# Kernel tuning notes

Measured on AMD Instinct MI355X. Metric: run time of the kernel, lower is better.

The kernel has to match this reference:

```python
import jax, jax.numpy as jnp
import numpy as np
from jax import lax

B, H, W, C = 64, 224, 224, 3
FLAT = 27040  # 52*52*10 after localization convs/pools


def conv_relu(x, w, b):
    y = lax.conv_general_dilated(x, w, (1, 1), 'VALID',
                                 dimension_numbers=('NHWC', 'HWIO', 'NHWC'))
    return jax.nn.relu(y + b)


def maxpool2(x):
    return lax.reduce_window(x, -jnp.inf, lax.max, (1, 2, 2, 1), (1, 2, 2, 1), 'VALID')


def affine_grid(h, w, theta):
    # normalized coords in [-1, 1]
    xt, yt = jnp.meshgrid(jnp.linspace(-1.0, 1.0, w), jnp.linspace(-1.0, 1.0, h))
    grid = jnp.stack([xt.ravel(), yt.ravel(), jnp.ones(h * w, theta.dtype)], 0)  # (3, h*w)
    g = jnp.einsum('bij,jp->bip', theta, grid)  # (B, 2, h*w)
    return g.reshape(-1, 2, h, w)


def bilinear_sampler(img, xs, ys):
    # xs, ys: (B, h, w) in [-1, 1]; img: (B, H, W, C)
    max_y, max_x = img.shape[1] - 1, img.shape[2] - 1
    x = 0.5 * (xs + 1.0) * max_x
    y = 0.5 * (ys + 1.0) * max_y
    x0 = jnp.clip(jnp.floor(x).astype(jnp.int32), 0, max_x)
    x1 = jnp.clip(x0 + 1, 0, max_x)
    y0 = jnp.clip(jnp.floor(y).astype(jnp.int32), 0, max_y)
    y1 = jnp.clip(y0 + 1, 0, max_y)
    b = jnp.arange(img.shape[0])[:, None, None]
    Ia = img[b, y0, x0]  # (B,h,w,C)
    Ib = img[b, y1, x0]
    Ic = img[b, y0, x1]
    Id = img[b, y1, x1]
    x0f, x1f = x0.astype(x.dtype), x1.astype(x.dtype)
    y0f, y1f = y0.astype(y.dtype), y1.astype(y.dtype)
    wa = ((x1f - x) * (y1f - y))[..., None]
    wb = ((x1f - x) * (y - y0f))[..., None]
    wc = ((x - x0f) * (y1f - y))[..., None]
    wd = ((x - x0f) * (y - y0f))[..., None]
    return wa * Ia + wb * Ib + wc * Ic + wd * Id


def setup_inputs() -> dict:
    key = jax.random.key(0)
    ks = jax.random.split(key, 6)
    inputs = jax.random.normal(ks[0], (B, H, W, C), jnp.float32)
    conv1_w = jax.random.normal(ks[1], (7, 7, 3, 8), jnp.float32) * (2.0 / (7 * 7 * 3)) ** 0.5
    conv1_b = jnp.zeros((8,), jnp.float32)
    conv2_w = jax.random.normal(ks[2], (5, 5, 8, 10), jnp.float32) * (2.0 / (5 * 5 * 8)) ** 0.5
    conv2_b = jnp.zeros((10,), jnp.float32)
    fc1_w = jax.random.normal(ks[3], (FLAT, 32), jnp.float32) * (2.0 / FLAT) ** 0.5
    fc1_b = jnp.zeros((32,), jnp.float32)
    fc2_w = jax.random.normal(ks[4], (32, 6), jnp.float32) * 0.01
    fc2_b = jnp.array([1, 0, 0, 0, 1, 0], jnp.float32)  # identity affine init
    return dict(inputs=inputs, conv1_w=conv1_w, conv1_b=conv1_b,
                conv2_w=conv2_w, conv2_b=conv2_b, fc1_w=fc1_w, fc1_b=fc1_b,
                fc2_w=fc2_w, fc2_b=fc2_b)


def reference(inputs, conv1_w, conv1_b, conv2_w, conv2_b, fc1_w, fc1_b, fc2_w, fc2_b):
    xs = maxpool2(conv_relu(inputs, conv1_w, conv1_b))
    xs = maxpool2(conv_relu(xs, conv2_w, conv2_b))
    xs = xs.reshape(xs.shape[0], -1)  # (B, 27040)
    h1 = jax.nn.relu(xs @ fc1_w + fc1_b)
    theta = (h1 @ fc2_w + fc2_b).reshape(-1, 2, 3)
    grid = affine_grid(H, W, theta)  # (B, 2, H, W)
    return bilinear_sampler(inputs, grid[:, 0], grid[:, 1])
```

## Files before the change

kernel.cpp:

```cpp
#include <hip/hip_runtime.h>


__global__ __launch_bounds__(256) void k_wcvt(
    const float* __restrict__ w1, const float* __restrict__ b1,
    const float* __restrict__ w2, const float* __restrict__ b2,
    double* __restrict__ wd) {
  int t = blockIdx.x * 256 + threadIdx.x;
  if (t < 1176) wd[t] = (double)w1[t];
  else if (t < 1184) wd[t] = (double)b1[t - 1176];
  else if (t < 3184) wd[t] = (double)w2[t - 1184];
  else if (t < 3194) wd[t] = (double)b2[t - 3184];
}

__global__ __launch_bounds__(448) void k_conv1(
    const float* __restrict__ in, const double* __restrict__ wd,
    double* __restrict__ out) {
  __shared__ float win[14 * 672];

  int g = blockIdx.x & 7;
  int i = blockIdx.x >> 3;
  int b = g * 8 + i / 28;
  int tile = i % 28;
  int py0 = 4 * tile;
  int r0 = 8 * tile;

  {
    const float* ibb = in + (size_t)b * 150528;
    for (int idx = threadIdx.x; idx < 14 * 168; idx += 448) {
      int rr = idx / 168, c4 = idx % 168;
      int row = min(r0 + rr, 223);
      float4 v = reinterpret_cast<const float4*>(ibb + (size_t)row * 672)[c4];
      reinterpret_cast<float4*>(&win[rr * 672])[c4] = v;
    }
  }
  __syncthreads();

  int t = threadIdx.x;
  int py = py0 + t / 109;
  if (t < 436 && py < 109) {
    int px = t % 109;
    int lrb = 2 * (t / 109);

    double acc[2][2][8];
#pragma unroll
    for (int ii = 0; ii < 2; ++ii)
#pragma unroll
      for (int j = 0; j < 2; ++j)
#pragma unroll
        for (int k = 0; k < 8; ++k) acc[ii][j][k] = 0.0;

    for (int ky = 0; ky < 7; ++ky) {
      const float* r0p = &win[(lrb + ky) * 672 + 6 * px];
      const float* r1p = r0p + 672;
      float a0[24], a1[24];
#pragma unroll
      for (int j = 0; j < 12; ++j) {
        float2 u = reinterpret_cast<const float2*>(r0p)[j];
        a0[2 * j] = u.x; a0[2 * j + 1] = u.y;
        float2 v = reinterpret_cast<const float2*>(r1p)[j];
        a1[2 * j] = v.x; a1[2 * j + 1] = v.y;
      }
      const double* wk = wd + ky * 168;
#pragma unroll
      for (int kx = 0; kx < 7; ++kx) {
#pragma unroll
        for (int c = 0; c < 3; ++c) {
          double v00 = (double)a0[kx * 3 + c];
          double v01 = (double)a0[kx * 3 + 3 + c];
          double v10 = (double)a1[kx * 3 + c];
          double v11 = (double)a1[kx * 3 + 3 + c];
          const double* wp = wk + (kx * 3 + c) * 8;
#pragma unroll
          for (int oc = 0; oc < 8; ++oc) {
            double wv = wp[oc];
            acc[0][0][oc] = fma(v00, wv, acc[0][0][oc]);
            acc[0][1][oc] = fma(v01, wv, acc[0][1][oc]);
            acc[1][0][oc] = fma(v10, wv, acc[1][0][oc]);
            acc[1][1][oc] = fma(v11, wv, acc[1][1][oc]);
          }
        }
      }
    }

    double* op = out + ((size_t)b * 11881 + (size_t)py * 109 + px) * 8;
#pragma unroll
    for (int oc = 0; oc < 8; ++oc) {
      double m = fmax(fmax(acc[0][0][oc], acc[0][1][oc]),
                      fmax(acc[1][0][oc], acc[1][1][oc]));
      op[oc] = fmax(m + wd[1176 + oc], 0.0);
    }
  }
}

__global__ __launch_bounds__(512) void k_conv2(
    const double* __restrict__ in, const double* __restrict__ wd2,
    double* __restrict__ out) {
  __shared__ double win2[4 * 12 * 2 * 56];

  int g = blockIdx.x & 7;
  int i = blockIdx.x >> 3;
  int b = g * 8 + i / 13;
  int tile = i % 13;
  int py0 = 4 * tile;
  int r0 = 8 * tile;

  int t = threadIdx.x;
  int oh = __builtin_amdgcn_readfirstlane(t >> 8);
  int p = t & 255;
  bool valid = p < 208;
  int px = p % 52;
  int lrb = 2 * (p / 52);

  const double* wb = wd2 + oh * 5;

  double acc[2][2][5];
#pragma unroll
  for (int ii = 0; ii < 2; ++ii)
#pragma unroll
    for (int jj = 0; jj < 2; ++jj)
#pragma unroll
      for (int k = 0; k < 5; ++k) acc[ii][jj][k] = 0.0;

  const double* ib = in + (size_t)b * 11881 * 8;

  for (int h = 0; h < 2; ++h) {
    __syncthreads();
    for (int idx = threadIdx.x; idx < 12 * 109 * 2; idx += 512) {
      int d2 = idx & 1;
      int x  = (idx >> 1) % 109;
      int rr = (idx >> 1) / 109;
      double2 v = *reinterpret_cast<const double2*>(
          ib + ((size_t)(r0 + rr) * 109 + x) * 8 + h * 4 + d2 * 2);
      int par = x & 1, k = x >> 1;
      win2[(((d2 * 2) * 12 + rr) * 2 + par) * 56 + k] = v.x;
      win2[(((d2 * 2 + 1) * 12 + rr) * 2 + par) * 56 + k] = v.y;
    }
    __syncthreads();

    if (valid) {
#pragma unroll
      for (int ky = 0; ky < 5; ++ky) {
        int rr0 = lrb + ky;
#pragma unroll
        for (int cc = 0; cc < 4; ++cc) {
          int c = h * 4 + cc;
          const double* pe0 = &win2[((cc * 12 + rr0) * 2 + 0) * 56 + px];
          const double* po0 = &win2[((cc * 12 + rr0) * 2 + 1) * 56 + px];
          const double* pe1 = pe0 + 112;
          const double* po1 = po0 + 112;
          double e0[3] = {pe0[0], pe0[1], pe0[2]};
          double o0[3] = {po0[0], po0[1], po0[2]};
          double e1[3] = {pe1[0], pe1[1], pe1[2]};
          double o1[3] = {po1[0], po1[1], po1[2]};
#pragma unroll
          for (int kx = 0; kx < 5; ++kx) {
            double v00, v01, v10, v11;
            if (kx & 1) {
              v00 = o0[kx >> 1]; v01 = e0[(kx >> 1) + 1];
              v10 = o1[kx >> 1]; v11 = e1[(kx >> 1) + 1];
            } else {
              v00 = e0[kx >> 1]; v01 = o0[kx >> 1];
              v10 = e1[kx >> 1]; v11 = o1[kx >> 1];
            }
            const double* wp = wb + ((ky * 5 + kx) * 8 + c) * 10;
#pragma unroll
            for (int oc = 0; oc < 5; ++oc) {
              double wv = wp[oc];
              acc[0][0][oc] = fma(v00, wv, acc[0][0][oc]);
              acc[0][1][oc] = fma(v01, wv, acc[0][1][oc]);
              acc[1][0][oc] = fma(v10, wv, acc[1][0][oc]);
              acc[1][1][oc] = fma(v11, wv, acc[1][1][oc]);
            }
          }
        }
      }
    }
  }

  if (valid) {
    int pix = py0 * 52 + p;
    double* op = out + ((size_t)b * 2704 + pix) * 10 + oh * 5;
#pragma unroll
    for (int oc = 0; oc < 5; ++oc) {
      double m = fmax(fmax(acc[0][0][oc], acc[0][1][oc]),
                      fmax(acc[1][0][oc], acc[1][1][oc]));
      op[oc] = fmax(m + wd2[2000 + oh * 5 + oc], 0.0);
    }
  }
}

__global__ __launch_bounds__(256) void k_fc1(
    const double* __restrict__ xs, const float* __restrict__ w1,
    double* __restrict__ part) {
  int b = blockIdx.x >> 4;
  int q = blockIdx.x & 15;
  int oc = threadIdx.x & 31;
  int s = threadIdx.x >> 5;
  const double* xrow = xs + (size_t)b * 27040;

  int i0 = q * 1690 + s * 212;
  int i1 = min(i0 + 212, q * 1690 + 1690);
  double s0 = 0.0, s1 = 0.0;
  for (int i = i0; i + 1 < i1; i += 2) {
    s0 = fma(xrow[i],     (double)w1[(size_t)i * 32 + oc],       s0);
    s1 = fma(xrow[i + 1], (double)w1[(size_t)(i + 1) * 32 + oc], s1);
  }
  if ((i1 - i0) & 1)
    s0 = fma(xrow[i1 - 1], (double)w1[(size_t)(i1 - 1) * 32 + oc], s0);

  __shared__ double red[8][32];
  red[s][oc] = s0 + s1;
  __syncthreads();
  if (threadIdx.x < 32) {
    double v = 0.0;
#pragma unroll
    for (int k = 0; k < 8; ++k) v += red[k][threadIdx.x];
    part[((size_t)b * 16 + q) * 32 + threadIdx.x] = v;
  }
}

__global__ __launch_bounds__(64) void k_fc2(
    const double* __restrict__ part, const float* __restrict__ b1,
    const float* __restrict__ w2, const float* __restrict__ b2,
    double* __restrict__ theta) {
  int b = blockIdx.x;
  __shared__ double h1[32];
  if (threadIdx.x < 32) {
    double v = (double)b1[threadIdx.x];
#pragma unroll
    for (int q = 0; q < 16; ++q)
      v += part[((size_t)b * 16 + q) * 32 + threadIdx.x];
    h1[threadIdx.x] = v > 0.0 ? v : 0.0;
  }
  __syncthreads();
  if (threadIdx.x < 6) {
    double v = (double)b2[threadIdx.x];
#pragma unroll
    for (int k = 0; k < 32; ++k) v += h1[k] * (double)w2[k * 6 + threadIdx.x];
    theta[b * 6 + threadIdx.x] = v;
  }
}

__global__ __launch_bounds__(256) void k_sample(
    const float* __restrict__ img, const double* __restrict__ theta,
    float* __restrict__ out) {
  int idx = blockIdx.x * 256 + threadIdx.x;
  if (idx >= 64 * 224 * 224) return;
  int x = idx % 224;
  int t = idx / 224;
  int y = t % 224;
  int b = t / 224;

  const double* th = theta + b * 6;
  double t0 = th[0], t1 = th[1], t2 = th[2];
  double t3 = th[3], t4 = th[4], t5 = th[5];

  double xn = -1.0 + x * (2.0 / 223.0);
  double yn = -1.0 + y * (2.0 / 223.0);
  double xf = 0.5 * (t0 * xn + t1 * yn + t2 + 1.0) * 223.0;
  double yf = 0.5 * (t3 * xn + t4 * yn + t5 + 1.0) * 223.0;

  int x0 = (int)floor(xf);
  int y0 = (int)floor(yf);
  x0 = min(max(x0, 0), 223);
  y0 = min(max(y0, 0), 223);
  int x1 = min(x0 + 1, 223);
  int y1 = min(y0 + 1, 223);

  double x0f = (double)x0, x1f = (double)x1;
  double y0f = (double)y0, y1f = (double)y1;
  double wa = (x1f - xf) * (y1f - yf);
  double wb = (x1f - xf) * (yf - y0f);
  double wc = (xf - x0f) * (y1f - yf);
  double wd = (xf - x0f) * (yf - y0f);

  const float* p = img + (size_t)b * 150528;
  const float* Ia = p + ((size_t)y0 * 224 + x0) * 3;
  const float* Ib = p + ((size_t)y1 * 224 + x0) * 3;
  const float* Ic = p + ((size_t)y0 * 224 + x1) * 3;
  const float* Id = p + ((size_t)y1 * 224 + x1) * 3;

  float* op = out + (size_t)idx * 3;
#pragma unroll
  for (int c = 0; c < 3; ++c) {
    op[c] = (float)(wa * (double)Ia[c] + wb * (double)Ib[c] +
                    wc * (double)Ic[c] + wd * (double)Id[c]);
  }
}

extern "C" void kernel_launch(void* const* d_in, const int* in_sizes, int n_in,
                              void* d_out, int out_size, void* d_ws, size_t ws_size,
                              hipStream_t stream) {
  const float* inputs  = (const float*)d_in[0];
  const float* conv1_w = (const float*)d_in[1];
  const float* conv1_b = (const float*)d_in[2];
  const float* conv2_w = (const float*)d_in[3];
  const float* conv2_b = (const float*)d_in[4];
  const float* fc1_w   = (const float*)d_in[5];
  const float* fc1_b   = (const float*)d_in[6];
  const float* fc2_w   = (const float*)d_in[7];
  const float* fc2_b   = (const float*)d_in[8];
  float* outp = (float*)d_out;

  double* theta = (double*)d_ws;
  double* part  = (double*)((char*)d_ws + 4096);
  double* wd    = (double*)((char*)d_ws + 4096 + 262144);
  double* pool1 = (double*)((char*)d_ws + 4096 + 262144 + 25600);
  double* pool2 = pool1 + 6083072;

  k_wcvt<<<13, 256, 0, stream>>>(conv1_w, conv1_b, conv2_w, conv2_b, wd);
  k_conv1<<<28 * 64, 448, 0, stream>>>(inputs, wd, pool1);
  k_conv2<<<13 * 64, 512, 0, stream>>>(pool1, wd + 1184, pool2);
  k_fc1<<<1024, 256, 0, stream>>>(pool2, fc1_w, part);
  k_fc2<<<64, 64, 0, stream>>>(part, fc1_b, fc2_w, fc2_b, theta);
  k_sample<<<(64 * 224 * 224 + 255) / 256, 256, 0, stream>>>(inputs, theta, outp);
}
```

Baseline: 394.3 us.

## Fuse fc1 and fc2 into one kernel and vectorize sampler output stores

Merges the split-K fc1 kernel and the fc2 kernel into a single 1024-thread block per batch that reduces partial sums in shared memory, removing one launch and the global partial-sum round trip. This also cuts fc1 parallelism from 1024 blocks to 64, so each block streams the full fc1 weight matrix with less latency hiding. The sampler now computes four adjacent output pixels per thread and writes them as three float4 stores, giving wider, coalesced writes at the cost of fewer threads.

After: 488.2 us. 23.8% more time.

```diff
diff --git a/kernel.cpp b/kernel.cpp
--- a/kernel.cpp
+++ b/kernel.cpp
@@ -189,47 +189,32 @@
   }
 }
 
-__global__ __launch_bounds__(256) void k_fc1(
+__global__ __launch_bounds__(1024) void k_fc(
     const double* __restrict__ xs, const float* __restrict__ w1,
-    double* __restrict__ part) {
-  int b = blockIdx.x >> 4;
-  int q = blockIdx.x & 15;
+    const float* __restrict__ b1, const float* __restrict__ w2,
+    const float* __restrict__ b2, double* __restrict__ theta) {
+  int b = blockIdx.x;
   int oc = threadIdx.x & 31;
   int s = threadIdx.x >> 5;
   const double* xrow = xs + (size_t)b * 27040;
 
-  int i0 = q * 1690 + s * 212;
-  int i1 = min(i0 + 212, q * 1690 + 1690);
+  int i0 = s * 845, i1 = i0 + 845;
   double s0 = 0.0, s1 = 0.0;
   for (int i = i0; i + 1 < i1; i += 2) {
     s0 = fma(xrow[i],     (double)w1[(size_t)i * 32 + oc],       s0);
     s1 = fma(xrow[i + 1], (double)w1[(size_t)(i + 1) * 32 + oc], s1);
   }
-  if ((i1 - i0) & 1)
-    s0 = fma(xrow[i1 - 1], (double)w1[(size_t)(i1 - 1) * 32 + oc], s0);
-
-  __shared__ double red[8][32];
+  s0 = fma(xrow[i1 - 1], (double)w1[(size_t)(i1 - 1) * 32 + oc], s0);
+
+  __shared__ double red[32][33];
   red[s][oc] = s0 + s1;
   __syncthreads();
-  if (threadIdx.x < 32) {
-    double v = 0.0;
-#pragma unroll
-    for (int k = 0; k < 8; ++k) v += red[k][threadIdx.x];
-    part[((size_t)b * 16 + q) * 32 + threadIdx.x] = v;
-  }
-}
-
-__global__ __launch_bounds__(64) void k_fc2(
-    const double* __restrict__ part, const float* __restrict__ b1,
-    const float* __restrict__ w2, const float* __restrict__ b2,
-    double* __restrict__ theta) {
-  int b = blockIdx.x;
+
   __shared__ double h1[32];
   if (threadIdx.x < 32) {
     double v = (double)b1[threadIdx.x];
 #pragma unroll
-    for (int q = 0; q < 16; ++q)
-      v += part[((size_t)b * 16 + q) * 32 + threadIdx.x];
+    for (int k = 0; k < 32; ++k) v += red[k][threadIdx.x];
     h1[threadIdx.x] = v > 0.0 ? v : 0.0;
   }
   __syncthreads();
@@ -244,48 +229,57 @@
 __global__ __launch_bounds__(256) void k_sample(
     const float* __restrict__ img, const double* __restrict__ theta,
     float* __restrict__ out) {
-  int idx = blockIdx.x * 256 + threadIdx.x;
-  if (idx >= 64 * 224 * 224) return;
-  int x = idx % 224;
-  int t = idx / 224;
-  int y = t % 224;
-  int b = t / 224;
+  int q = blockIdx.x * 256 + threadIdx.x;
+  if (q >= 64 * 224 * 56) return;
+  int xg = q % 56;
+  int ty = q / 56;
+  int y = ty % 224;
+  int b = ty / 224;
 
   const double* th = theta + b * 6;
   double t0 = th[0], t1 = th[1], t2 = th[2];
   double t3 = th[3], t4 = th[4], t5 = th[5];
 
-  double xn = -1.0 + x * (2.0 / 223.0);
   double yn = -1.0 + y * (2.0 / 223.0);
-  double xf = 0.5 * (t0 * xn + t1 * yn + t2 + 1.0) * 223.0;
-  double yf = 0.5 * (t3 * xn + t4 * yn + t5 + 1.0) * 223.0;
-
-  int x0 = (int)floor(xf);
-  int y0 = (int)floor(yf);
-  x0 = min(max(x0, 0), 223);
-  y0 = min(max(y0, 0), 223);
-  int x1 = min(x0 + 1, 223);
-  int y1 = min(y0 + 1, 223);
-
-  double x0f = (double)x0, x1f = (double)x1;
-  double y0f = (double)y0, y1f = (double)y1;
-  double wa = (x1f - xf) * (y1f - yf);
-  double wb = (x1f - xf) * (yf - y0f);
-  double wc = (xf - x0f) * (y1f - yf);
-  double wd = (xf - x0f) * (yf - y0f);
-
   const float* p = img + (size_t)b * 150528;
-  const float* Ia = p + ((size_t)y0 * 224 + x0) * 3;
-  const float* Ib = p + ((size_t)y1 * 224 + x0) * 3;
-  const float* Ic = p + ((size_t)y0 * 224 + x1) * 3;
-  const float* Id = p + ((size_t)y1 * 224 + x1) * 3;
-
-  float* op = out + (size_t)idx * 3;
-#pragma unroll
-  for (int c = 0; c < 3; ++c) {
-    op[c] = (float)(wa * (double)Ia[c] + wb * (double)Ib[c] +
-                    wc * (double)Ic[c] + wd * (double)Id[c]);
-  }
+
+  float ov[12];
+#pragma unroll
+  for (int j = 0; j < 4; ++j) {
+    int x = xg * 4 + j;
+    double xn = -1.0 + x * (2.0 / 223.0);
+    double xf = 0.5 * (t0 * xn + t1 * yn + t2 + 1.0) * 223.0;
+    double yf = 0.5 * (t3 * xn + t4 * yn + t5 + 1.0) * 223.0;
+
+    int x0 = (int)floor(xf);
+    int y0 = (int)floor(yf);
+    x0 = min(max(x0, 0), 223);
+    y0 = min(max(y0, 0), 223);
+    int x1 = min(x0 + 1, 223);
+    int y1 = min(y0 + 1, 223);
+
+    double x0f = (double)x0, x1f = (double)x1;
+    double y0f = (double)y0, y1f = (double)y1;
+    double wa = (x1f - xf) * (y1f - yf);
+    double wb = (x1f - xf) * (yf - y0f);
+    double wc = (xf - x0f) * (y1f - yf);
+    double wd = (xf - x0f) * (yf - y0f);
+
+    const float* Ia = p + ((size_t)y0 * 224 + x0) * 3;
+    const float* Ib = p + ((size_t)y1 * 224 + x0) * 3;
+    const float* Ic = p + ((size_t)y0 * 224 + x1) * 3;
+    const float* Id = p + ((size_t)y1 * 224 + x1) * 3;
+#pragma unroll
+    for (int c = 0; c < 3; ++c) {
+      ov[j * 3 + c] = (float)(wa * (double)Ia[c] + wb * (double)Ib[c] +
+                              wc * (double)Ic[c] + wd * (double)Id[c]);
+    }
+  }
+
+  float4* op = reinterpret_cast<float4*>(out + ((size_t)ty * 224 + xg * 4) * 3);
+  op[0] = make_float4(ov[0], ov[1], ov[2], ov[3]);
+  op[1] = make_float4(ov[4], ov[5], ov[6], ov[7]);
+  op[2] = make_float4(ov[8], ov[9], ov[10], ov[11]);
 }
 
 extern "C" void kernel_launch(void* const* d_in, const int* in_sizes, int n_in,
@@ -303,7 +297,6 @@
   float* outp = (float*)d_out;
 
   double* theta = (double*)d_ws;
-  double* part  = (double*)((char*)d_ws + 4096);
   double* wd    = (double*)((char*)d_ws + 4096 + 262144);
   double* pool1 = (double*)((char*)d_ws + 4096 + 262144 + 25600);
   double* pool2 = pool1 + 6083072;
@@ -311,7 +304,6 @@
   k_wcvt<<<13, 256, 0, stream>>>(conv1_w, conv1_b, conv2_w, conv2_b, wd);
   k_conv1<<<28 * 64, 448, 0, stream>>>(inputs, wd, pool1);
   k_conv2<<<13 * 64, 512, 0, stream>>>(pool1, wd + 1184, pool2);
-  k_fc1<<<1024, 256, 0, stream>>>(pool2, fc1_w, part);
-  k_fc2<<<64, 64, 0, stream>>>(part, fc1_b, fc2_w, fc2_b, theta);
-  k_sample<<<(64 * 224 * 224 + 255) / 256, 256, 0, stream>>>(inputs, theta, outp);
-}
+  k_fc<<<64, 1024, 0, stream>>>(pool2, fc1_w, fc1_b, fc2_w, fc2_b, theta);
+  k_sample<<<(64 * 224 * 56 + 255) / 256, 256, 0, stream>>>(inputs, theta, outp);
+}
```
